# Performance work log

Measured on AMD Instinct MI355X. Metric: run time of the kernel, lower is better.

Reference implementation:

```python
import jax, jax.numpy as jnp
import numpy as np
import math

D = 2048
H = 16
DH = D // H
DFF = 8192
B = 4
S = 2048
EPS = 1e-12


def gelu(x):
    # faithful tanh-approx gelu from source
    return 0.5 * x * (1.0 + jnp.tanh(math.sqrt(2.0 / math.pi) * (x + 0.044715 * x ** 3)))


def global_layernorm(x, w, b):
    # torch.mean(x)/torch.var(x): scalar mean and UNBIASED variance over ALL elements
    mean = jnp.mean(x)
    var = jnp.var(x, ddof=1)
    return (x - mean) / jnp.sqrt(var + EPS) * w + b


def setup_inputs() -> dict:
    key = jax.random.key(0)
    ks = jax.random.split(key, 12)
    sd = 0.02
    return {
        "x": jax.random.normal(ks[0], (B, S, D), jnp.float32),
        "W1_w": jax.random.normal(ks[1], (3 * D, D), jnp.float32) * sd,
        "W1_b": jnp.zeros((3 * D,), jnp.float32),
        "W2_w": jax.random.normal(ks[2], (D, D), jnp.float32) * sd,
        "W2_b": jnp.zeros((D,), jnp.float32),
        "fc_w": jax.random.normal(ks[3], (DFF, D), jnp.float32) * sd,
        "fc_b": jnp.zeros((DFF,), jnp.float32),
        "proj_w": jax.random.normal(ks[4], (D, DFF), jnp.float32) * sd,
        "proj_b": jnp.zeros((D,), jnp.float32),
        "ln1_w": jnp.ones((D,), jnp.float32),
        "ln1_b": jnp.zeros((D,), jnp.float32),
        "ln2_w": jnp.ones((D,), jnp.float32),
        "ln2_b": jnp.zeros((D,), jnp.float32),
    }


def attn(x, W1_w, W1_b, W2_w, W2_b):
    X = x @ W1_w.T + W1_b                     # [B,S,3D]
    Q, K, V = jnp.split(X, 3, axis=2)         # each [B,S,D]
    # reshape(): view (B,S,H,Dh) then permute
    q = Q.reshape(B, S, H, DH).transpose(0, 2, 3, 1)  # [B,H,Dh,S]
    k = K.reshape(B, S, H, DH).transpose(0, 2, 1, 3)  # [B,H,S,Dh]
    v = V.reshape(B, S, H, DH).transpose(0, 2, 3, 1)  # [B,H,Dh,S]
    # heads(): scores over head-feature dim, scaled by sqrt(q.size(-1)) = sqrt(S)
    w = jnp.einsum('bhds,bhse->bhde', q, k) / math.sqrt(S)  # [B,H,Dh,Dh]
    w = jax.nn.softmax(w, axis=-1)
    out = jnp.einsum('bhde,bhes->bhds', w, v)  # [B,H,Dh,S]
    # cat(): raw contiguous view [B,H,Dh,S] -> [B,S,H*Dh] (memory-order reshape)
    out = out.reshape(B, S, H * DH)
    return out @ W2_w.T + W2_b


def ffn(x, fc_w, fc_b, proj_w, proj_b):
    h = gelu(x @ fc_w.T + fc_b)
    return h @ proj_w.T + proj_b


def reference(x, W1_w, W1_b, W2_w, W2_b, fc_w, fc_b, proj_w, proj_b,
              ln1_w, ln1_b, ln2_w, ln2_b):
    a = attn(x, W1_w, W1_b, W2_w, W2_b)
    x = global_layernorm(a + x, ln1_w, ln1_b)
    m = ffn(x, fc_w, fc_b, proj_w, proj_b)
    x = global_layernorm(m + x, ln2_w, ln2_b)
    return x
```

## Files before the change

kernel.cpp:

```cpp
#include <hip/hip_runtime.h>
#include <math.h>

typedef float floatx4 __attribute__((ext_vector_type(4)));
typedef __bf16 bf16x8 __attribute__((ext_vector_type(8)));
typedef unsigned short ushortx8 __attribute__((ext_vector_type(8)));
typedef unsigned short ushortx4 __attribute__((ext_vector_type(4)));
typedef unsigned short ushortx2 __attribute__((ext_vector_type(2)));

typedef unsigned int __attribute__((address_space(1))) as1_uint;
typedef unsigned int __attribute__((address_space(3))) as3_uint;

#define DEV static __device__ __forceinline__

DEV unsigned short f32_bf16(float f) {
  unsigned u = __float_as_uint(f);
  u += 0x7FFFu + ((u >> 16) & 1u);
  return (unsigned short)(u >> 16);
}
DEV float bf16_f32(unsigned short h) { return __uint_as_float(((unsigned)h) << 16); }
DEV float gelu_f(float x) {
  float t2 = 1.5957691216057308f * (x + 0.044715f * x * x * x);
  return x * __builtin_amdgcn_rcpf(1.0f + __expf(-t2));
}
DEV void gload16(const void* g, void* l) {
  __builtin_amdgcn_global_load_lds((const as1_uint*)g, (as3_uint*)l, 16, 0, 0);
}
DEV floatx4 mfma16(ushortx8 a, ushortx8 b, floatx4 c) {
  return __builtin_amdgcn_mfma_f32_16x16x32_bf16(
      __builtin_bit_cast(bf16x8, a), __builtin_bit_cast(bf16x8, b), c, 0, 0, 0);
}


__global__ void zero_f(float* p, int n) {
  int i = threadIdx.x;
  if (i < n) p[i] = 0.f;
}

__global__ void cvt_f32_bf16(const float* __restrict__ in, unsigned short* __restrict__ out,
                             long n4) {
  long i = (long)blockIdx.x * blockDim.x + threadIdx.x;
  if (i >= n4) return;
  float4 v = ((const float4*)in)[i];
  ushortx4 o;
  o.x = f32_bf16(v.x); o.y = f32_bf16(v.y); o.z = f32_bf16(v.z); o.w = f32_bf16(v.w);
  ((ushortx4*)out)[i] = o;
}

__global__ void cvt_cols(const float* __restrict__ in, unsigned short* __restrict__ out,
                         int cbase, int cwlog4, long n4) {
  long i = (long)blockIdx.x * blockDim.x + threadIdx.x;
  if (i >= n4) return;
  int n = (int)(i >> cwlog4);
  int k4 = (int)(i & ((1 << cwlog4) - 1)) << 2;
  float4 v = *(const float4*)&in[(size_t)n * 8192 + cbase + k4];
  ushortx4 o;
  o.x = f32_bf16(v.x); o.y = f32_bf16(v.y); o.z = f32_bf16(v.z); o.w = f32_bf16(v.w);
  *(ushortx4*)&out[((size_t)n << (cwlog4 + 2)) + k4] = o;
}

__global__ __launch_bounds__(256) void softmax_k(const float* __restrict__ sc,
                                                 unsigned short* __restrict__ probs) {
  int r = blockIdx.x * 4 + (threadIdx.x >> 6);
  int lane = threadIdx.x & 63;
  size_t base = (size_t)(r >> 7) * 16384 + (size_t)(r & 127) * 128 + lane * 2;
  float2 p0 = *(const float2*)&sc[base];
  float2 p1 = *(const float2*)&sc[base + 1048576];
  float2 p2 = *(const float2*)&sc[base + 2097152];
  float2 p3 = *(const float2*)&sc[base + 3145728];
  const float scale = 0.022097086912079608f;
  float vx = (p0.x + p1.x + p2.x + p3.x) * scale;
  float vy = (p0.y + p1.y + p2.y + p3.y) * scale;
  float m = fmaxf(vx, vy);
#pragma unroll
  for (int off = 32; off; off >>= 1) m = fmaxf(m, __shfl_xor(m, off));
  float ex = expf(vx - m), ey = expf(vy - m);
  float s = ex + ey;
#pragma unroll
  for (int off = 32; off; off >>= 1) s += __shfl_xor(s, off);
  float inv = 1.f / s;
  ushortx2 o;
  o.x = f32_bf16(ex * inv);
  o.y = f32_bf16(ey * inv);
  *(ushortx2*)&probs[base] = o;
}

__global__ void ln_apply(const float* __restrict__ r, const float* __restrict__ stats,
                         const float* __restrict__ w, const float* __restrict__ bia,
                         float* __restrict__ outF, unsigned short* __restrict__ outB, long n4) {
  long i = (long)blockIdx.x * blockDim.x + threadIdx.x;
  if (i >= n4) return;
  const double total = 16777216.0;
  double mean = (double)stats[0] / total;
  double var = ((double)stats[1] - total * mean * mean) / (total - 1.0);
  float rstd = (float)(1.0 / sqrt(var + 1e-12));
  float fm = (float)mean;
  int col = (int)((i * 4) & 2047);
  float4 v = ((const float4*)r)[i];
  float4 wv = *(const float4*)&w[col];
  float4 bv = *(const float4*)&bia[col];
  float4 o;
  o.x = (v.x - fm) * rstd * wv.x + bv.x;
  o.y = (v.y - fm) * rstd * wv.y + bv.y;
  o.z = (v.z - fm) * rstd * wv.z + bv.z;
  o.w = (v.w - fm) * rstd * wv.w + bv.w;
  if (outF) ((float4*)outF)[i] = o;
  if (outB) {
    ushortx4 ob;
    ob.x = f32_bf16(o.x); ob.y = f32_bf16(o.y); ob.z = f32_bf16(o.z); ob.w = f32_bf16(o.w);
    ((ushortx4*)outB)[i] = ob;
  }
}

__global__ __launch_bounds__(256) void gemm_bt(
    const unsigned short* __restrict__ A, int lda, long sAo, long sAi,
    const unsigned short* __restrict__ B, int ldb, long sBo, long sBi,
    int K, int innerCnt,
    const float* __restrict__ bias, const float* __restrict__ residF,
    const unsigned short* __restrict__ residB, int accum,
    float* __restrict__ outF, unsigned short* __restrict__ outB,
    unsigned short* __restrict__ outQT,
    int ldc, long sCo, long sCi, int doGelu, float* __restrict__ stats) {
  __shared__ unsigned short As[128 * 64];
  __shared__ unsigned short Bs[128 * 64];
  const int tid = threadIdx.x;
  const int wave = tid >> 6;
  const int lane = tid & 63;
  const int z = blockIdx.z;
  const int zo = z / innerCnt, zi = z % innerCnt;
  const unsigned short* Ab = A + zo * sAo + zi * sAi;
  const unsigned short* Bb = B + zo * sBo + zi * sBi;
  const long coff = zo * sCo + zi * sCi;
  const int m0 = blockIdx.y * 128;
  const int n0 = blockIdx.x * 128;

  const int quad = lane >> 4;
  const int l16 = lane & 15;
  const int wm = (wave & 1) * 64;
  const int wn = (wave >> 1) * 64;
  const int srow = lane >> 3;
  const int kofs8 = (((lane & 7) ^ srow) & 7) * 8;

  floatx4 acc[4][4];
#pragma unroll
  for (int i = 0; i < 4; i++)
#pragma unroll
    for (int j = 0; j < 4; j++) acc[i][j] = (floatx4){0.f, 0.f, 0.f, 0.f};

  const int nK = K >> 6;
  for (int kt = 0; kt < nK; ++kt) {
    const int k0 = kt << 6;
    __syncthreads();
#pragma unroll
    for (int i = 0; i < 4; ++i) {
      const int rb = wave * 32 + i * 8;
      gload16(Ab + (size_t)(m0 + rb + srow) * lda + k0 + kofs8, &As[rb * 64]);
      gload16(Bb + (size_t)(n0 + rb + srow) * ldb + k0 + kofs8, &Bs[rb * 64]);
    }
    __syncthreads();
#pragma unroll
    for (int kk = 0; kk < 2; ++kk) {
      ushortx8 af[4], bf[4];
      const int swz = (l16 & 7);
#pragma unroll
      for (int i = 0; i < 4; i++)
        af[i] = *(const ushortx8*)&As[(wm + i * 16 + l16) * 64 +
                                      (((kk * 4 + quad) ^ swz) * 8)];
#pragma unroll
      for (int j = 0; j < 4; j++)
        bf[j] = *(const ushortx8*)&Bs[(wn + j * 16 + l16) * 64 +
                                      (((kk * 4 + quad) ^ swz) * 8)];
#pragma unroll
      for (int i = 0; i < 4; i++)
#pragma unroll
        for (int j = 0; j < 4; j++) acc[i][j] = mfma16(af[i], bf[j], acc[i][j]);
    }
  }

  float s1 = 0.f, s2 = 0.f;
#pragma unroll
  for (int i = 0; i < 4; i++) {
#pragma unroll
    for (int j = 0; j < 4; j++) {
      const int col = n0 + wn + j * 16 + l16;
      const float bv = bias ? bias[col] : 0.f;
#pragma unroll
      for (int r = 0; r < 4; r++) {
        const int row = m0 + wm + i * 16 + quad * 4 + r;
        float v = acc[i][j][r] + bv;
        if (doGelu) v = gelu_f(v);
        if (outQT) {
          const int b = row >> 11, s = row & 2047;
          if (col < 4096) {
            unsigned short* tb = outQT + ((col & 2048) ? 16777216u : 0u);
            const int cc = col & 2047;
            tb[((size_t)((b << 4) + (cc >> 7)) * 128 + (cc & 127)) * 2048 + s] = f32_bf16(v);
          } else {
            outB[(size_t)row * 2048 + (col - 4096)] = f32_bf16(v);
          }
          continue;
        }
        const size_t cidx = (size_t)coff + (size_t)row * ldc + col;
        if (residF) v += residF[cidx];
        if (residB) v += bf16_f32(residB[cidx]);
        if (accum) v += outF[cidx];
        if (outF) outF[cidx] = v;
        else outB[cidx] = f32_bf16(v);
        if (stats) { s1 += v; s2 += v * v; }
      }
    }
  }
  if (stats) {
#pragma unroll
    for (int off = 32; off; off >>= 1) {
      s1 += __shfl_down(s1, off);
      s2 += __shfl_down(s2, off);
    }
    if (lane == 0) {
      atomicAdd(&stats[0], s1);
      atomicAdd(&stats[1], s2);
    }
  }
}

__global__ __launch_bounds__(512, 2) void gemm256(
    const unsigned short* __restrict__ A, int lda,
    const unsigned short* __restrict__ B, int ldb, int K,
    const float* __restrict__ bias, const float* __restrict__ residF,
    const unsigned short* __restrict__ residB, int accum,
    float* __restrict__ outF, unsigned short* __restrict__ outB,
    unsigned short* __restrict__ outQT, int ldc, int doGelu,
    float* __restrict__ stats) {
  __shared__ unsigned short As[2][256 * 64];
  __shared__ unsigned short Bs[2][256 * 64];
  const int tid = threadIdx.x;
  const int wave = tid >> 6;
  const int lane = tid & 63;
  const int wm = wave >> 2;
  const int wn = wave & 3;
  const int quad = lane >> 4;
  const int l16 = lane & 15;
  const int swz = l16 & 7;

  const int nwg = gridDim.x * gridDim.y;
  const int orig = blockIdx.y * gridDim.x + blockIdx.x;
  const int q8 = nwg >> 3, r8 = nwg & 7;
  const int xcd = orig & 7, lid = orig >> 3;
  const int wgid = (xcd < r8 ? xcd * (q8 + 1) : r8 * (q8 + 1) + (xcd - r8) * q8) + lid;
  int m0, n0;
  if ((gridDim.x & 7) == 0) {
    const int gper = (int)(gridDim.y << 3);
    m0 = ((wgid % gper) >> 3) * 256;
    n0 = (((wgid / gper) << 3) + (wgid & 7)) * 256;
  } else {
    m0 = (wgid / gridDim.x) * 256;
    n0 = (wgid % gridDim.x) * 256;
  }

  const int srow = lane >> 3;
  const int kof = (((lane & 7) ^ srow) & 7) << 3;
  const int nkt = K >> 6;

  floatx4 acc[8][4];
#pragma unroll
  for (int i = 0; i < 8; i++)
#pragma unroll
    for (int j = 0; j < 4; j++) acc[i][j] = (floatx4){0.f, 0.f, 0.f, 0.f};

  auto slot = [&](int kt, int s) {
    const int buf = kt & 1;
    const int k0 = kt << 6;
    if (s < 2) {
      const int rb = s * 128 + wave * 16;
      gload16(B + (size_t)(n0 + rb + srow) * ldb + k0 + kof, &Bs[buf][rb * 64]);
      gload16(B + (size_t)(n0 + rb + 8 + srow) * ldb + k0 + kof, &Bs[buf][(rb + 8) * 64]);
    } else {
      const int rb = ((wave & 4) << 5) + ((wave & 3) << 4) + (s == 3 ? 64 : 0);
      gload16(A + (size_t)(m0 + rb + srow) * lda + k0 + kof, &As[buf][rb * 64]);
      gload16(A + (size_t)(m0 + rb + 8 + srow) * lda + k0 + kof, &As[buf][(rb + 8) * 64]);
    }
  };

  slot(0, 0); slot(0, 1); slot(0, 2); slot(0, 3);
  if (nkt > 1) { slot(1, 0); slot(1, 1); slot(1, 2); }
  asm volatile("s_waitcnt vmcnt(6)" ::: "memory");
  __builtin_amdgcn_s_barrier();
  asm volatile("" ::: "memory");

  ushortx8 bfr[4][2], afr[2][2];
  const int aBase = (wm * 128 + l16) * 64;
  const int bBase = (wn * 64 + l16) * 64;
  const int kq0 = (quad ^ swz) << 3;
  const int kq1 = ((4 + quad) ^ swz) << 3;

  for (int kt = 0; kt < nkt; kt += 2) {
    const int m2 = (kt + 2 < nkt);
    const int m3 = (kt + 3 < nkt);
#pragma unroll
    for (int half = 0; half < 2; half++) {
      const unsigned short* Asb = &As[half][0];
      const unsigned short* Bsb = &Bs[half][0];
#pragma unroll
      for (int p = 0; p < 4; p++) {
        if (p == 0) {
#pragma unroll
          for (int fj = 0; fj < 4; fj++) {
            bfr[fj][0] = *(const ushortx8*)&Bsb[bBase + fj * 1024 + kq0];
            bfr[fj][1] = *(const ushortx8*)&Bsb[bBase + fj * 1024 + kq1];
          }
        }
#pragma unroll
        for (int fi = 0; fi < 2; fi++) {
          afr[fi][0] = *(const ushortx8*)&Asb[aBase + (p * 2 + fi) * 1024 + kq0];
          afr[fi][1] = *(const ushortx8*)&Asb[aBase + (p * 2 + fi) * 1024 + kq1];
        }
        if (half == 0) {
          if (p == 0) { if (kt + 1 < nkt) slot(kt + 1, 3); }
          else if (m2) slot(kt + 2, p - 1);
        } else {
          if (p == 0) { if (m2) slot(kt + 2, 3); }
          else if (m3) slot(kt + 3, p - 1);
        }
        asm volatile("" ::: "memory");
        __builtin_amdgcn_s_barrier();
        asm volatile("" ::: "memory");
        __builtin_amdgcn_s_setprio(1);
#pragma unroll
        for (int fi = 0; fi < 2; fi++)
#pragma unroll
          for (int fj = 0; fj < 4; fj++) {
            acc[p * 2 + fi][fj] = mfma16(afr[fi][0], bfr[fj][0], acc[p * 2 + fi][fj]);
            acc[p * 2 + fi][fj] = mfma16(afr[fi][1], bfr[fj][1], acc[p * 2 + fi][fj]);
          }
        __builtin_amdgcn_s_setprio(0);
        if (p == 1) {
          if (half == 0) {
            if (m2) asm volatile("s_waitcnt vmcnt(10)" ::: "memory");
            else    asm volatile("s_waitcnt vmcnt(8)" ::: "memory");
          } else {
            if (m3) asm volatile("s_waitcnt vmcnt(10)" ::: "memory");
            else    asm volatile("s_waitcnt vmcnt(0)" ::: "memory");
          }
        } else if (p == 3) {
          if (half == 0) {
            if (m2) asm volatile("s_waitcnt vmcnt(8)" ::: "memory");
            else    asm volatile("s_waitcnt vmcnt(2)" ::: "memory");
          } else {
            if (m3) asm volatile("s_waitcnt vmcnt(8)" ::: "memory");
            else    asm volatile("s_waitcnt vmcnt(0)" ::: "memory");
          }
        }
        asm volatile("" ::: "memory");
        __builtin_amdgcn_s_barrier();
        asm volatile("" ::: "memory");
      }
    }
  }

  if (outQT) {
    if (n0 < 4096) {
      unsigned short* trb = (wave < 4) ? (unsigned short*)&As[0][0] + wave * 8192
                                       : (unsigned short*)&Bs[0][0] + (wave - 4) * 8192;
#pragma unroll
      for (int j = 0; j < 4; j++) {
        const int c = j * 16 + l16;
        const float bv = bias ? bias[n0 + wn * 64 + c] : 0.f;
#pragma unroll
        for (int i = 0; i < 8; i++) {
          ushortx4 o;
          o.x = f32_bf16(acc[i][j][0] + bv);
          o.y = f32_bf16(acc[i][j][1] + bv);
          o.z = f32_bf16(acc[i][j][2] + bv);
          o.w = f32_bf16(acc[i][j][3] + bv);
          *(ushortx4*)&trb[c * 128 + (((i * 4 + quad) ^ (c & 6)) << 2)] = o;
        }
      }
      const int bb = m0 >> 11;
      const int sbase = (m0 & 2047) + wm * 128;
      unsigned short* tb = outQT + ((n0 & 2048) ? 16777216u : 0u);
      const int cg = lane >> 4;
      const int sl = lane & 15;
#pragma unroll
      for (int it = 0; it < 16; it++) {
        const int c = it * 4 + cg;
        ushortx8 v = *(const ushortx8*)&trb[c * 128 + (((2 * sl) ^ (c & 6)) << 2)];
        const int cc = (n0 + wn * 64 + c) & 2047;
        unsigned short* dst = tb +
            ((size_t)((bb << 4) + (cc >> 7)) * 128 + (cc & 127)) * 2048 + sbase + sl * 8;
        *(ushortx8*)dst = v;
      }
    } else {
#pragma unroll
      for (int i = 0; i < 8; i++)
#pragma unroll
        for (int j = 0; j < 4; j++) {
          const int col = n0 + wn * 64 + j * 16 + l16;
          const float bv = bias ? bias[col] : 0.f;
#pragma unroll
          for (int r = 0; r < 4; r++) {
            const int row = m0 + wm * 128 + i * 16 + quad * 4 + r;
            outB[(size_t)row * 2048 + (col - 4096)] = f32_bf16(acc[i][j][r] + bv);
          }
        }
    }
    return;
  }

  float s1 = 0.f, s2 = 0.f;
#pragma unroll
  for (int i = 0; i < 8; i++) {
#pragma unroll
    for (int j = 0; j < 4; j++) {
      const int col = n0 + wn * 64 + j * 16 + l16;
      const float bv = bias ? bias[col] : 0.f;
#pragma unroll
      for (int r = 0; r < 4; r++) {
        const int row = m0 + wm * 128 + i * 16 + quad * 4 + r;
        float v = acc[i][j][r] + bv;
        if (doGelu) v = gelu_f(v);
        const size_t cidx = (size_t)row * ldc + col;
        if (residF) v += residF[cidx];
        if (residB) v += bf16_f32(residB[cidx]);
        if (accum) v += outF[cidx];
        if (outF) outF[cidx] = v;
        else outB[cidx] = f32_bf16(v);
        if (stats) { s1 += v; s2 += v * v; }
      }
    }
  }
  if (stats) {
#pragma unroll
    for (int off = 32; off; off >>= 1) {
      s1 += __shfl_down(s1, off);
      s2 += __shfl_down(s2, off);
    }
    if (lane == 0) {
      atomicAdd(&stats[0], s1);
      atomicAdd(&stats[1], s2);
    }
  }
}


extern "C" void kernel_launch(void* const* d_in, const int* in_sizes, int n_in, void* d_out,
                              int out_size, void* d_ws, size_t ws_size, hipStream_t stream) {
  (void)in_sizes; (void)n_in; (void)out_size;
  const float* x    = (const float*)d_in[0];
  const float* W1w  = (const float*)d_in[1];
  const float* W1b  = (const float*)d_in[2];
  const float* W2w  = (const float*)d_in[3];
  const float* W2b  = (const float*)d_in[4];
  const float* fcw  = (const float*)d_in[5];
  const float* fcb  = (const float*)d_in[6];
  const float* pjw  = (const float*)d_in[7];
  const float* pjb  = (const float*)d_in[8];
  const float* ln1w = (const float*)d_in[9];
  const float* ln1b = (const float*)d_in[10];
  const float* ln2w = (const float*)d_in[11];
  const float* ln2b = (const float*)d_in[12];
  float* out = (float*)d_out;

  char* ws = (char*)d_ws;
  size_t off = 0;
  auto take = [&](size_t b) { size_t r = off; off = (off + b + 255) & ~(size_t)255; return r; };
  float* stats = (float*)(ws + take(256));
  size_t P0 = take(33554432);
  size_t P1 = take(25165824);
  size_t P2 = take(100663296);
  size_t P3 = off;

  unsigned short* xbf    = (unsigned short*)(ws + P0);
  unsigned short* attnbf = (unsigned short*)(ws + P0);
  unsigned short* W1bf   = (unsigned short*)(ws + P1);
  float*          spart  = (float*)(ws + P1);
  unsigned short* probs  = (unsigned short*)(ws + P1 + 16777216);
  unsigned short* W2bf   = (unsigned short*)(ws + P1);
  unsigned short* vbf    = (unsigned short*)(ws + P2);
  unsigned short* qT     = (unsigned short*)(ws + P2 + 33554432);
  float*          r12    = (float*)(ws + P2);
  unsigned short* x1bf   = (unsigned short*)(ws + P2 + 67108864);

  int nc;
  unsigned short *fc_ch, *pj_ch, *hch;
  if (ws_size >= P3 + 201326592) {
    nc = 1;
    fc_ch = (unsigned short*)(ws + P3);
    pj_ch = (unsigned short*)(ws + P3 + 33554432);
    hch   = (unsigned short*)(ws + P3 + 67108864);
  } else if (ws_size >= P3 + 100663296) {
    nc = 2;
    fc_ch = (unsigned short*)(ws + P3);
    pj_ch = (unsigned short*)(ws + P3 + 16777216);
    hch   = (unsigned short*)(ws + P3 + 33554432);
  } else {
    nc = 4;
    fc_ch = (unsigned short*)(ws + P1);
    pj_ch = (unsigned short*)(ws + P1 + 8388608);
    hch   = (unsigned short*)(ws + P0);
  }
  const int cw = 8192 / nc;
  const int cwlog4 = (nc == 1) ? 11 : (nc == 2) ? 10 : 9;
  const long cn4 = (long)cw << 9;

  zero_f<<<1, 64, 0, stream>>>(stats, 16);
  cvt_f32_bf16<<<16384, 256, 0, stream>>>(x, xbf, 4194304);
  cvt_f32_bf16<<<12288, 256, 0, stream>>>(W1w, W1bf, 3145728);

  gemm256<<<dim3(24, 32, 1), 512, 0, stream>>>(xbf, 2048, W1bf, 2048, 2048, W1b, nullptr,
                                               nullptr, 0, nullptr, vbf, qT, 0, 0, nullptr);
  gemm_bt<<<dim3(1, 1, 256), 256, 0, stream>>>(qT, 2048, 262144L, 512L, qT + 16777216, 2048,
                                               262144L, 512L, 512, 4, nullptr, nullptr, nullptr,
                                               0, spart, nullptr, nullptr, 128, 16384L, 1048576L,
                                               0, nullptr);
  softmax_k<<<2048, 256, 0, stream>>>(spart, probs);
  gemm_bt<<<dim3(16, 1, 64), 256, 0, stream>>>(probs, 128, 262144L, 16384L, vbf, 2048, 4194304L,
                                               128L, 128, 16, nullptr, nullptr, nullptr, 0,
                                               nullptr, attnbf, nullptr, 2048, 4194304L, 262144L,
                                               0, nullptr);
  cvt_f32_bf16<<<4096, 256, 0, stream>>>(W2w, W2bf, 1048576);
  gemm256<<<dim3(8, 32, 1), 512, 0, stream>>>(attnbf, 2048, W2bf, 2048, 2048, W2b, x, nullptr,
                                              0, r12, nullptr, nullptr, 2048, 0, stats);
  ln_apply<<<16384, 256, 0, stream>>>(r12, stats, ln1w, ln1b, nullptr, x1bf, 4194304);

  for (int c = 0; c < nc; ++c) {
    cvt_f32_bf16<<<(int)(cn4 / 256), 256, 0, stream>>>(fcw + (size_t)c * cw * 2048, fc_ch, cn4);
    cvt_cols<<<(int)(cn4 / 256), 256, 0, stream>>>(pjw, pj_ch, c * cw, cwlog4, cn4);
    gemm256<<<dim3(cw / 256, 32, 1), 512, 0, stream>>>(x1bf, 2048, fc_ch, 2048, 2048,
                                                       fcb + c * cw, nullptr, nullptr, 0,
                                                       nullptr, hch, nullptr, cw, 1, nullptr);
    const int last = (c == nc - 1);
    gemm256<<<dim3(8, 32, 1), 512, 0, stream>>>(hch, cw, pj_ch, cw, cw,
                                                last ? pjb : nullptr, nullptr,
                                                last ? x1bf : nullptr, c > 0, r12, nullptr,
                                                nullptr, 2048, 0,
                                                last ? (stats + 2) : nullptr);
  }
  ln_apply<<<16384, 256, 0, stream>>>(r12, stats + 2, ln2w, ln2b, out, nullptr, 4194304);
}
```

Before: 1.346 ms.

## Restructure GEMM main loop into explicit unrolled ping-pong stages with lgkmcnt waits

```diff
diff --git a/kernel.cpp b/kernel.cpp
--- a/kernel.cpp
+++ b/kernel.cpp
@@ -230,8 +230,10 @@
     float* __restrict__ outF, unsigned short* __restrict__ outB,
     unsigned short* __restrict__ outQT, int ldc, int doGelu,
     float* __restrict__ stats) {
-  __shared__ unsigned short As[2][256 * 64];
-  __shared__ unsigned short Bs[2][256 * 64];
+  __shared__ unsigned short As0[256 * 64];
+  __shared__ unsigned short As1[256 * 64];
+  __shared__ unsigned short Bs0[256 * 64];
+  __shared__ unsigned short Bs1[256 * 64];
   const int tid = threadIdx.x;
   const int wave = tid >> 6;
   const int lane = tid & 63;
@@ -266,25 +268,18 @@
 #pragma unroll
     for (int j = 0; j < 4; j++) acc[i][j] = (floatx4){0.f, 0.f, 0.f, 0.f};
 
-  auto slot = [&](int kt, int s) {
-    const int buf = kt & 1;
+  auto stageB = [&](unsigned short* dst, int kt, int s) {
     const int k0 = kt << 6;
-    if (s < 2) {
-      const int rb = s * 128 + wave * 16;
-      gload16(B + (size_t)(n0 + rb + srow) * ldb + k0 + kof, &Bs[buf][rb * 64]);
-      gload16(B + (size_t)(n0 + rb + 8 + srow) * ldb + k0 + kof, &Bs[buf][(rb + 8) * 64]);
-    } else {
-      const int rb = ((wave & 4) << 5) + ((wave & 3) << 4) + (s == 3 ? 64 : 0);
-      gload16(A + (size_t)(m0 + rb + srow) * lda + k0 + kof, &As[buf][rb * 64]);
-      gload16(A + (size_t)(m0 + rb + 8 + srow) * lda + k0 + kof, &As[buf][(rb + 8) * 64]);
-    }
+    const int rb = s * 128 + wave * 16;
+    gload16(B + (size_t)(n0 + rb + srow) * ldb + k0 + kof, &dst[rb * 64]);
+    gload16(B + (size_t)(n0 + rb + 8 + srow) * ldb + k0 + kof, &dst[(rb + 8) * 64]);
   };
-
-  slot(0, 0); slot(0, 1); slot(0, 2); slot(0, 3);
-  if (nkt > 1) { slot(1, 0); slot(1, 1); slot(1, 2); }
-  asm volatile("s_waitcnt vmcnt(6)" ::: "memory");
-  __builtin_amdgcn_s_barrier();
-  asm volatile("" ::: "memory");
+  auto stageA = [&](unsigned short* dst, int kt, int hi) {
+    const int k0 = kt << 6;
+    const int rb = ((wave & 4) << 5) + ((wave & 3) << 4) + hi * 64;
+    gload16(A + (size_t)(m0 + rb + srow) * lda + k0 + kof, &dst[rb * 64]);
+    gload16(A + (size_t)(m0 + rb + 8 + srow) * lda + k0 + kof, &dst[(rb + 8) * 64]);
+  };
 
   ushortx8 bfr[4][2], afr[2][2];
   const int aBase = (wm * 128 + l16) * 64;
@@ -292,74 +287,90 @@
   const int kq0 = (quad ^ swz) << 3;
   const int kq1 = ((4 + quad) ^ swz) << 3;
 
+  auto rdB = [&](const unsigned short* Bsb) {
+#pragma unroll
+    for (int fj = 0; fj < 4; fj++) {
+      bfr[fj][0] = *(const ushortx8*)&Bsb[bBase + fj * 1024 + kq0];
+      bfr[fj][1] = *(const ushortx8*)&Bsb[bBase + fj * 1024 + kq1];
+    }
+  };
+  auto rdA = [&](const unsigned short* Asb, int p) {
+#pragma unroll
+    for (int fi = 0; fi < 2; fi++) {
+      afr[fi][0] = *(const ushortx8*)&Asb[aBase + (p * 2 + fi) * 1024 + kq0];
+      afr[fi][1] = *(const ushortx8*)&Asb[aBase + (p * 2 + fi) * 1024 + kq1];
+    }
+  };
+  auto mma = [&](int p) {
+    __builtin_amdgcn_s_setprio(1);
+#pragma unroll
+    for (int fi = 0; fi < 2; fi++)
+#pragma unroll
+      for (int fj = 0; fj < 4; fj++) {
+        acc[p * 2 + fi][fj] = mfma16(afr[fi][0], bfr[fj][0], acc[p * 2 + fi][fj]);
+        acc[p * 2 + fi][fj] = mfma16(afr[fi][1], bfr[fj][1], acc[p * 2 + fi][fj]);
+      }
+    __builtin_amdgcn_s_setprio(0);
+  };
+
+#define BAR() __builtin_amdgcn_s_barrier()
+#define LGKM0()                                            \
+  do {                                                     \
+    asm volatile("s_waitcnt lgkmcnt(0)" ::: "memory");     \
+    __builtin_amdgcn_sched_barrier(0);                     \
+  } while (0)
+#define LGKM8() asm volatile("s_waitcnt lgkmcnt(8)" ::: "memory")
+#define VM6() asm volatile("s_waitcnt vmcnt(6)" ::: "memory")
+#define VM0() asm volatile("s_waitcnt vmcnt(0)" ::: "memory")
+
+  stageB(Bs0, 0, 0); stageB(Bs0, 0, 1); stageA(As0, 0, 0); stageA(As0, 0, 1);
+  if (nkt > 1) { stageB(Bs1, 1, 0); stageB(Bs1, 1, 1); stageA(As1, 1, 0); }
+  VM6();
+  BAR();
+
   for (int kt = 0; kt < nkt; kt += 2) {
-    const int m2 = (kt + 2 < nkt);
-    const int m3 = (kt + 3 < nkt);
-#pragma unroll
-    for (int half = 0; half < 2; half++) {
-      const unsigned short* Asb = &As[half][0];
-      const unsigned short* Bsb = &Bs[half][0];
-#pragma unroll
-      for (int p = 0; p < 4; p++) {
-        if (p == 0) {
-#pragma unroll
-          for (int fj = 0; fj < 4; fj++) {
-            bfr[fj][0] = *(const ushortx8*)&Bsb[bBase + fj * 1024 + kq0];
-            bfr[fj][1] = *(const ushortx8*)&Bsb[bBase + fj * 1024 + kq1];
-          }
-        }
-#pragma unroll
-        for (int fi = 0; fi < 2; fi++) {
-          afr[fi][0] = *(const ushortx8*)&Asb[aBase + (p * 2 + fi) * 1024 + kq0];
-          afr[fi][1] = *(const ushortx8*)&Asb[aBase + (p * 2 + fi) * 1024 + kq1];
-        }
-        if (half == 0) {
-          if (p == 0) { if (kt + 1 < nkt) slot(kt + 1, 3); }
-          else if (m2) slot(kt + 2, p - 1);
-        } else {
-          if (p == 0) { if (m2) slot(kt + 2, 3); }
-          else if (m3) slot(kt + 3, p - 1);
-        }
-        asm volatile("" ::: "memory");
-        __builtin_amdgcn_s_barrier();
-        asm volatile("" ::: "memory");
-        __builtin_amdgcn_s_setprio(1);
-#pragma unroll
-        for (int fi = 0; fi < 2; fi++)
-#pragma unroll
-          for (int fj = 0; fj < 4; fj++) {
-            acc[p * 2 + fi][fj] = mfma16(afr[fi][0], bfr[fj][0], acc[p * 2 + fi][fj]);
-            acc[p * 2 + fi][fj] = mfma16(afr[fi][1], bfr[fj][1], acc[p * 2 + fi][fj]);
-          }
-        __builtin_amdgcn_s_setprio(0);
-        if (p == 1) {
-          if (half == 0) {
-            if (m2) asm volatile("s_waitcnt vmcnt(10)" ::: "memory");
-            else    asm volatile("s_waitcnt vmcnt(8)" ::: "memory");
-          } else {
-            if (m3) asm volatile("s_waitcnt vmcnt(10)" ::: "memory");
-            else    asm volatile("s_waitcnt vmcnt(0)" ::: "memory");
-          }
-        } else if (p == 3) {
-          if (half == 0) {
-            if (m2) asm volatile("s_waitcnt vmcnt(8)" ::: "memory");
-            else    asm volatile("s_waitcnt vmcnt(2)" ::: "memory");
-          } else {
-            if (m3) asm volatile("s_waitcnt vmcnt(8)" ::: "memory");
-            else    asm volatile("s_waitcnt vmcnt(0)" ::: "memory");
-          }
-        }
-        asm volatile("" ::: "memory");
-        __builtin_amdgcn_s_barrier();
-        asm volatile("" ::: "memory");
-      }
-    }
-  }
+    const bool t2 = kt + 2 < nkt, t3 = kt + 3 < nkt;
+    rdB(Bs0); rdA(As0, 0);
+    if (kt + 1 < nkt) stageA(As1, kt + 1, 1);
+    LGKM8();
+    BAR(); LGKM0(); mma(0); BAR();
+
+    rdA(As0, 1); if (t2) stageB(Bs0, kt + 2, 0);
+    BAR(); LGKM0(); mma(1); BAR();
+
+    rdA(As0, 2); if (t2) stageB(Bs0, kt + 2, 1);
+    BAR(); LGKM0(); mma(2); BAR();
+
+    rdA(As0, 3); if (t2) stageA(As0, kt + 2, 0);
+    BAR(); LGKM0(); mma(3);
+    if (t2) VM6(); else VM0();
+    BAR();
+
+    rdB(Bs1); rdA(As1, 0);
+    if (t2) stageA(As0, kt + 2, 1);
+    LGKM8();
+    BAR(); LGKM0(); mma(0); BAR();
+
+    rdA(As1, 1); if (t3) stageB(Bs1, kt + 3, 0);
+    BAR(); LGKM0(); mma(1); BAR();
+
+    rdA(As1, 2); if (t3) stageB(Bs1, kt + 3, 1);
+    BAR(); LGKM0(); mma(2); BAR();
+
+    rdA(As1, 3); if (t3) stageA(As1, kt + 3, 0);
+    BAR(); LGKM0(); mma(3);
+    if (t3) VM6();
+    BAR();
+  }
+#undef BAR
+#undef LGKM0
+#undef LGKM8
+#undef VM6
+#undef VM0
 
   if (outQT) {
     if (n0 < 4096) {
-      unsigned short* trb = (wave < 4) ? (unsigned short*)&As[0][0] + wave * 8192
-                                       : (unsigned short*)&Bs[0][0] + (wave - 4) * 8192;
+      unsigned short* trb = (wave < 4) ? As0 + wave * 8192 : Bs0 + (wave - 4) * 8192;
 #pragma unroll
       for (int j = 0; j < 4; j++) {
         const int c = j * 16 + l16;
```

After: 1.342 ms. About the same (-0.3%).
